# Kernel tuning notes

Measured on AMD Instinct MI355X. Metric: run time of the kernel, lower is better.

## Reference

```python
import jax, jax.numpy as jnp
import numpy as np

N = 50000
F = 128
E = 800000
HOP = 3
ALPHA = 0.2  # leaky relu slope


def setup_inputs() -> dict:
    key = jax.random.key(0)
    ks = jax.random.split(key, 6)
    x = jax.random.normal(ks[0], (N, F), dtype=jnp.float32)
    h0 = jax.random.normal(ks[1], (N, F), dtype=jnp.float32)
    edge_index = jax.random.randint(ks[2], (2, E), 0, N, dtype=jnp.int32)
    edge_weight = jax.random.uniform(ks[3], (E,), dtype=jnp.float32)
    # xavier-uniform-ish params
    lim_w = float(np.sqrt(6.0 / (F + F)))
    W_att = jax.random.uniform(ks[4], (F, F), dtype=jnp.float32, minval=-lim_w, maxval=lim_w)
    lim_a = 1.414 * float(np.sqrt(6.0 / (2 * F + 1)))
    a = jax.random.uniform(ks[5], (2 * F, 1), dtype=jnp.float32, minval=-lim_a, maxval=lim_a)
    temp = jnp.zeros((4,), dtype=jnp.float32)
    return {"x": x, "h0": h0, "edge_index": edge_index, "edge_weight": edge_weight,
            "W_att": W_att, "a": a, "temp": temp}


def _segment_softmax(e, rows, num_segments):
    m = jax.ops.segment_max(e, rows, num_segments=num_segments)
    m = jnp.where(jnp.isfinite(m), m, 0.0)  # guard empty rows
    ex = jnp.exp(e - m[rows])
    s = jax.ops.segment_sum(ex, rows, num_segments=num_segments)
    s = jnp.where(s > 0, s, 1.0)
    return ex / s[rows]


def reference(x, h0, edge_index, edge_weight, W_att, a, temp):
    rows, cols = edge_index[0], edge_index[1]
    # --- attention (edge-wise, never materializing dense NxN e) ---
    feat = x @ W_att                       # [N, F]
    f1 = (feat @ a[:F]).squeeze(-1)        # [N]
    f2 = (feat @ a[F:]).squeeze(-1)        # [N]
    e = f1[rows] + f2[cols]                # e[i,j] at edges
    e = jnp.where(e > 0, e, ALPHA * e)     # leaky relu
    att = _segment_softmax(e, rows, N)     # sparse row softmax values
    P = 0.5 * att
    # --- lifting bases ---
    coe = jax.nn.sigmoid(temp)
    rowsum = jax.ops.segment_sum(edge_weight * P, rows, num_segments=N)  # [N]
    update = x
    feat_prime = None
    for step in range(HOP):
        # sparse mm: U @ update
        update = jax.ops.segment_sum(att[:, None] * update[cols], rows, num_segments=N)
        feat_even = coe[0] * x + update
        feat_odd = update - feat_even * rowsum[:, None]
        feat_prime = feat_odd if step == 0 else coe[2] * feat_prime + (1.0 - coe[2]) * feat_odd
    return feat_prime
```

## Files before the change

### kernel.cpp

```cpp
#include <hip/hip_runtime.h>
#include <hip/hip_fp16.h>

#define NN 50000
#define FF 128
#define EE 800000
#define CAP 48
#define ALPHA 0.2f
#define ESHIFT 4.0f

__global__ void k_w(const float* __restrict__ W, const float* __restrict__ a,
                    float* __restrict__ w12) {
    int k = threadIdx.x;
    float s1 = 0.f, s2 = 0.f;
    const float* wr = W + k * FF;
    for (int j = 0; j < FF; ++j) {
        float w = wr[j];
        s1 += w * a[j];
        s2 += w * a[FF + j];
    }
    w12[k] = s1;
    w12[FF + k] = s2;
}

__global__ void k_f(const float* __restrict__ x, const float* __restrict__ w12,
                    float* __restrict__ f1, float* __restrict__ f2,
                    __half* __restrict__ xh) {
    int gid = blockIdx.x * blockDim.x + threadIdx.x;
    int node = gid >> 6;
    int lane = threadIdx.x & 63;
    if (node >= NN) return;
    float2 xv = ((const float2*)(x + (size_t)node * FF))[lane];
    ((__half2*)(xh + (size_t)node * FF))[lane] = __float22half2_rn(xv);
    float2 w1 = ((const float2*)w12)[lane];
    float2 w2 = ((const float2*)(w12 + FF))[lane];
    float s1 = xv.x * w1.x + xv.y * w1.y;
    float s2 = xv.x * w2.x + xv.y * w2.y;
#pragma unroll
    for (int o = 32; o > 0; o >>= 1) {
        s1 += __shfl_down(s1, o);
        s2 += __shfl_down(s2, o);
    }
    if (lane == 0) { f1[node] = s1; f2[node] = s2; }
}

__global__ void k_edge(const int* __restrict__ rows, const int* __restrict__ cols,
                       const float* __restrict__ ew, const float* __restrict__ f1,
                       const float* __restrict__ f2, int* __restrict__ fill,
                       int2* __restrict__ bucket) {
    const int STR = EE / 4;
    int t = blockIdx.x * blockDim.x + threadIdx.x;
    if (t >= STR) return;
    int r[4], c[4];
    float w[4];
#pragma unroll
    for (int k = 0; k < 4; ++k) {
        int e = t + k * STR;
        r[k] = rows[e];
        c[k] = cols[e];
        w[k] = ew[e];
    }
    float f1v[4], f2v[4];
#pragma unroll
    for (int k = 0; k < 4; ++k) { f1v[k] = f1[r[k]]; f2v[k] = f2[c[k]]; }
    int pay[4];
#pragma unroll
    for (int k = 0; k < 4; ++k) {
        float v = f1v[k] + f2v[k];
        v = v > 0.f ? v : ALPHA * v;
        float ex = __expf(v - ESHIFT);
        union { int i; __half2 h; } p;
        p.h = __floats2half2_rn(ex, w[k] * ex);
        pay[k] = p.i;
    }
    int pos[4];
#pragma unroll
    for (int k = 0; k < 4; ++k) pos[k] = atomicAdd(&fill[r[k]], 1);
#pragma unroll
    for (int k = 0; k < 4; ++k) {
        if (pos[k] < CAP)
            bucket[(size_t)r[k] * CAP + pos[k]] = make_int2(c[k], pay[k]);
    }
}

__global__ void k_hop(const float* __restrict__ x, const __half* __restrict__ uin,
                      __half* __restrict__ uout, const int* __restrict__ fill,
                      const int2* __restrict__ bucket, const float* __restrict__ temp,
                      __half* __restrict__ S, float* __restrict__ out, int step) {
    int wave = threadIdx.x >> 6;
    int lane = threadIdx.x & 63;
    int r = __builtin_amdgcn_readfirstlane(blockIdx.x * 4 + wave);
    if (r >= NN) return;
    int d = fill[r];
    if (d > CAP) d = CAP;
    const int2* bk = bucket + (size_t)r * CAP;
    float ax = 0.f, ay = 0.f, se = 0.f, sw = 0.f;
    int j = 0;
    for (; j + 8 <= d; j += 8) {
        int2 b[8];
        __half2 h[8];
#pragma unroll
        for (int t = 0; t < 8; ++t) b[t] = bk[j + t];
#pragma unroll
        for (int t = 0; t < 8; ++t)
            h[t] = ((const __half2*)(uin + (size_t)b[t].x * FF))[lane];
#pragma unroll
        for (int t = 0; t < 8; ++t) {
            union { int i; __half2 h2; } p;
            p.i = b[t].y;
            float2 ee = __half22float2(p.h2);
            float2 u = __half22float2(h[t]);
            ax += ee.x * u.x;
            ay += ee.x * u.y;
            se += ee.x;
            sw += ee.y;
        }
    }
    for (; j < d; ++j) {
        int2 b = bk[j];
        __half2 hv = ((const __half2*)(uin + (size_t)b.x * FF))[lane];
        union { int i; __half2 h2; } p;
        p.i = b.y;
        float2 ee = __half22float2(p.h2);
        float2 u = __half22float2(hv);
        ax += ee.x * u.x;
        ay += ee.x * u.y;
        se += ee.x;
        sw += ee.y;
    }
    float inv = se > 0.f ? 1.f / se : 0.f;
    ax *= inv;
    ay *= inv;
    float c2 = 1.f / (1.f + __expf(-temp[2]));
    __half2* Sr = (__half2*)(S + (size_t)r * FF);
    if (step == 0) {
        ((__half2*)(uout + (size_t)r * FF))[lane] = __float22half2_rn(make_float2(ax, ay));
        float w0 = c2 * c2;
        Sr[lane] = __float22half2_rn(make_float2(w0 * ax, w0 * ay));
    } else if (step == 1) {
        ((__half2*)(uout + (size_t)r * FF))[lane] = __float22half2_rn(make_float2(ax, ay));
        float w1 = c2 * (1.f - c2);
        float2 sv = __half22float2(Sr[lane]);
        Sr[lane] = __float22half2_rn(make_float2(sv.x + w1 * ax, sv.y + w1 * ay));
    } else {
        float rs = 0.5f * sw * inv;
        float coe0 = 1.f / (1.f + __expf(-temp[0]));
        float w2 = 1.f - c2;
        float2 sv = __half22float2(Sr[lane]);
        float2 xv = ((const float2*)(x + (size_t)r * FF))[lane];
        float k1 = 1.f - rs;
        float k2 = coe0 * rs;
        ((float2*)(out + (size_t)r * FF))[lane] =
            make_float2(k1 * (sv.x + w2 * ax) - k2 * xv.x,
                        k1 * (sv.y + w2 * ay) - k2 * xv.y);
    }
}

extern "C" void kernel_launch(void* const* d_in, const int* in_sizes, int n_in,
                              void* d_out, int out_size, void* d_ws, size_t ws_size,
                              hipStream_t stream) {
    const float* x = (const float*)d_in[0];
    const int* eidx = (const int*)d_in[2];
    const int* rows = eidx;
    const int* cols = eidx + EE;
    const float* ew = (const float*)d_in[3];
    const float* W = (const float*)d_in[4];
    const float* a = (const float*)d_in[5];
    const float* temp = (const float*)d_in[6];
    float* out = (float*)d_out;

    float* ws = (float*)d_ws;
    int* fill = (int*)ws;
    float* f1 = ws + NN;
    float* f2 = ws + 2 * NN;
    float* w12 = ws + 3 * NN;
    int2* bucket = (int2*)(ws + 3 * NN + 256);
    __half* xh = (__half*)(bucket + (size_t)NN * CAP);
    __half* uh0 = xh + (size_t)NN * FF;
    __half* Sb = uh0 + (size_t)NN * FF;
    __half* uh1 = xh;

    hipMemsetAsync(fill, 0, NN * sizeof(int), stream);

    k_w<<<1, 128, 0, stream>>>(W, a, w12);
    k_f<<<(NN + 3) / 4, 256, 0, stream>>>(x, w12, f1, f2, xh);
    k_edge<<<(EE / 4 + 255) / 256, 256, 0, stream>>>(rows, cols, ew, f1, f2, fill, bucket);
    k_hop<<<(NN + 3) / 4, 256, 0, stream>>>(x, xh, uh0, fill, bucket, temp, Sb, out, 0);
    k_hop<<<(NN + 3) / 4, 256, 0, stream>>>(x, uh0, uh1, fill, bucket, temp, Sb, out, 1);
    k_hop<<<(NN + 3) / 4, 256, 0, stream>>>(x, uh1, nullptr, fill, bucket, temp, Sb, out, 2);
}
```

Baseline: 283.9 us.

## Build compact CSR via two-level binning instead of per-row atomic buckets

Result: faster. 258.4 us (-9.0%).

```diff
diff --git a/kernel.cpp b/kernel.cpp
--- a/kernel.cpp
+++ b/kernel.cpp
@@ -4,9 +4,13 @@
 #define NN 50000
 #define FF 128
 #define EE 800000
-#define CAP 48
 #define ALPHA 0.2f
 #define ESHIFT 4.0f
+
+#define NBINS 196
+#define RPB 256
+#define CAPB 5120
+#define EPB 2048
 
 __global__ void k_w(const float* __restrict__ W, const float* __restrict__ a,
                     float* __restrict__ w12) {
@@ -43,56 +47,122 @@
     if (lane == 0) { f1[node] = s1; f2[node] = s2; }
 }
 
-__global__ void k_edge(const int* __restrict__ rows, const int* __restrict__ cols,
-                       const float* __restrict__ ew, const float* __restrict__ f1,
-                       const float* __restrict__ f2, int* __restrict__ fill,
-                       int2* __restrict__ bucket) {
-    const int STR = EE / 4;
-    int t = blockIdx.x * blockDim.x + threadIdx.x;
-    if (t >= STR) return;
-    int r[4], c[4];
-    float w[4];
-#pragma unroll
-    for (int k = 0; k < 4; ++k) {
-        int e = t + k * STR;
-        r[k] = rows[e];
-        c[k] = cols[e];
-        w[k] = ew[e];
-    }
-    float f1v[4], f2v[4];
-#pragma unroll
-    for (int k = 0; k < 4; ++k) { f1v[k] = f1[r[k]]; f2v[k] = f2[c[k]]; }
-    int pay[4];
-#pragma unroll
-    for (int k = 0; k < 4; ++k) {
-        float v = f1v[k] + f2v[k];
-        v = v > 0.f ? v : ALPHA * v;
-        float ex = __expf(v - ESHIFT);
-        union { int i; __half2 h; } p;
-        p.h = __floats2half2_rn(ex, w[k] * ex);
-        pay[k] = p.i;
-    }
-    int pos[4];
-#pragma unroll
-    for (int k = 0; k < 4; ++k) pos[k] = atomicAdd(&fill[r[k]], 1);
-#pragma unroll
-    for (int k = 0; k < 4; ++k) {
-        if (pos[k] < CAP)
-            bucket[(size_t)r[k] * CAP + pos[k]] = make_int2(c[k], pay[k]);
-    }
+__global__ void k_bin(const int* __restrict__ rows, const int* __restrict__ cols,
+                      const float* __restrict__ ew, const float* __restrict__ f1,
+                      const float* __restrict__ f2, int* __restrict__ bin_fill,
+                      int2* __restrict__ binbuf) {
+    __shared__ int cnt[NBINS];
+    __shared__ int gbase[NBINS];
+    int tid = threadIdx.x;
+    if (tid < NBINS) cnt[tid] = 0;
+    __syncthreads();
+    int e0 = blockIdx.x * EPB;
+    int rk[8], bn[8], rc[8], pay[8];
+    bool vl[8];
+#pragma unroll
+    for (int k = 0; k < 8; ++k) {
+        int e = e0 + k * 256 + tid;
+        vl[k] = e < EE;
+        if (vl[k]) {
+            int r = rows[e], c = cols[e];
+            float v = f1[r] + f2[c];
+            v = v > 0.f ? v : ALPHA * v;
+            float ex = __expf(v - ESHIFT);
+            union { int i; __half2 h; } p;
+            p.h = __floats2half2_rn(ex, ew[e] * ex);
+            pay[k] = p.i;
+            rc[k] = (r << 16) | c;
+            bn[k] = r >> 8;
+            rk[k] = atomicAdd(&cnt[bn[k]], 1);
+        }
+    }
+    __syncthreads();
+    if (tid < NBINS) {
+        int c0 = cnt[tid];
+        gbase[tid] = c0 ? atomicAdd(&bin_fill[tid], c0) : 0;
+    }
+    __syncthreads();
+#pragma unroll
+    for (int k = 0; k < 8; ++k) {
+        if (vl[k]) {
+            int pos = gbase[bn[k]] + rk[k];
+            if (pos < CAPB) binbuf[(size_t)bn[k] * CAPB + pos] = make_int2(rc[k], pay[k]);
+        }
+    }
+}
+
+__global__ void k_csr(const int* __restrict__ bin_fill, const int2* __restrict__ binbuf,
+                      int2* __restrict__ csr, int* __restrict__ row_ptr) {
+    __shared__ int sc[256];
+    __shared__ int lfill[RPB];
+    __shared__ int2 grouped[CAPB];
+    int tid = threadIdx.x;
+    int bin = blockIdx.x;
+    if (tid < 256) {
+        int v = (tid < NBINS) ? bin_fill[tid] : 0;
+        sc[tid] = v > CAPB ? CAPB : v;
+    }
+    __syncthreads();
+    for (int s = 1; s < 256; s <<= 1) {
+        int t = 0;
+        if (tid < 256) t = sc[tid] + (tid >= s ? sc[tid - s] : 0);
+        __syncthreads();
+        if (tid < 256) sc[tid] = t;
+        __syncthreads();
+    }
+    int base = (bin > 0) ? sc[bin - 1] : 0;
+    int cnt = sc[bin] - base;
+    __syncthreads();
+    if (tid < RPB) lfill[tid] = 0;
+    __syncthreads();
+    int2 ent[5];
+    int rnk[5], rl[5];
+    bool vl[5];
+#pragma unroll
+    for (int it = 0; it < 5; ++it) {
+        int i = tid + it * 1024;
+        vl[it] = i < cnt;
+        if (vl[it]) {
+            ent[it] = binbuf[(size_t)bin * CAPB + i];
+            rl[it] = (((unsigned)ent[it].x) >> 16) & 0xFF;
+            rnk[it] = atomicAdd(&lfill[rl[it]], 1);
+        }
+    }
+    __syncthreads();
+    if (tid < 256) sc[tid] = lfill[tid];
+    __syncthreads();
+    for (int s = 1; s < 256; s <<= 1) {
+        int t = 0;
+        if (tid < 256) t = sc[tid] + (tid >= s ? sc[tid - s] : 0);
+        __syncthreads();
+        if (tid < 256) sc[tid] = t;
+        __syncthreads();
+    }
+#pragma unroll
+    for (int it = 0; it < 5; ++it) {
+        if (vl[it])
+            grouped[sc[rl[it]] - lfill[rl[it]] + rnk[it]] =
+                make_int2(ent[it].x & 0xFFFF, ent[it].y);
+    }
+    __syncthreads();
+    for (int i = tid; i < cnt; i += 1024) csr[base + i] = grouped[i];
+    int r0 = bin << 8;
+    int nrows = NN - r0 < RPB ? NN - r0 : RPB;
+    if (tid < nrows) row_ptr[r0 + tid] = base + sc[tid] - lfill[tid];
+    if (bin == NBINS - 1 && tid == 0) row_ptr[NN] = base + cnt;
 }
 
 __global__ void k_hop(const float* __restrict__ x, const __half* __restrict__ uin,
-                      __half* __restrict__ uout, const int* __restrict__ fill,
-                      const int2* __restrict__ bucket, const float* __restrict__ temp,
+                      __half* __restrict__ uout, const int* __restrict__ row_ptr,
+                      const int2* __restrict__ csr, const float* __restrict__ temp,
                       __half* __restrict__ S, float* __restrict__ out, int step) {
     int wave = threadIdx.x >> 6;
     int lane = threadIdx.x & 63;
     int r = __builtin_amdgcn_readfirstlane(blockIdx.x * 4 + wave);
     if (r >= NN) return;
-    int d = fill[r];
-    if (d > CAP) d = CAP;
-    const int2* bk = bucket + (size_t)r * CAP;
+    int beg = row_ptr[r], end = row_ptr[r + 1];
+    const int2* bk = csr + beg;
+    int d = end - beg;
     float ax = 0.f, ay = 0.f, se = 0.f, sw = 0.f;
     int j = 0;
     for (; j + 8 <= d; j += 8) {
@@ -169,22 +239,25 @@
     float* out = (float*)d_out;
 
     float* ws = (float*)d_ws;
-    int* fill = (int*)ws;
-    float* f1 = ws + NN;
-    float* f2 = ws + 2 * NN;
-    float* w12 = ws + 3 * NN;
-    int2* bucket = (int2*)(ws + 3 * NN + 256);
-    __half* xh = (__half*)(bucket + (size_t)NN * CAP);
+    int* bin_fill = (int*)ws;
+    float* w12 = ws + 256;
+    float* f1 = ws + 512;
+    float* f2 = f1 + NN;
+    int* row_ptr = (int*)(f2 + NN);
+    int2* csr = (int2*)(row_ptr + NN + 64);
+    __half* xh = (__half*)(csr + EE);
     __half* uh0 = xh + (size_t)NN * FF;
     __half* Sb = uh0 + (size_t)NN * FF;
+    int2* binbuf = (int2*)Sb;
     __half* uh1 = xh;
 
-    hipMemsetAsync(fill, 0, NN * sizeof(int), stream);
+    hipMemsetAsync(bin_fill, 0, NBINS * sizeof(int), stream);
 
     k_w<<<1, 128, 0, stream>>>(W, a, w12);
     k_f<<<(NN + 3) / 4, 256, 0, stream>>>(x, w12, f1, f2, xh);
-    k_edge<<<(EE / 4 + 255) / 256, 256, 0, stream>>>(rows, cols, ew, f1, f2, fill, bucket);
-    k_hop<<<(NN + 3) / 4, 256, 0, stream>>>(x, xh, uh0, fill, bucket, temp, Sb, out, 0);
-    k_hop<<<(NN + 3) / 4, 256, 0, stream>>>(x, uh0, uh1, fill, bucket, temp, Sb, out, 1);
-    k_hop<<<(NN + 3) / 4, 256, 0, stream>>>(x, uh1, nullptr, fill, bucket, temp, Sb, out, 2);
-}
+    k_bin<<<(EE + EPB - 1) / EPB, 256, 0, stream>>>(rows, cols, ew, f1, f2, bin_fill, binbuf);
+    k_csr<<<NBINS, 1024, 0, stream>>>(bin_fill, binbuf, csr, row_ptr);
+    k_hop<<<(NN + 3) / 4, 256, 0, stream>>>(x, xh, uh0, row_ptr, csr, temp, Sb, out, 0);
+    k_hop<<<(NN + 3) / 4, 256, 0, stream>>>(x, uh0, uh1, row_ptr, csr, temp, Sb, out, 1);
+    k_hop<<<(NN + 3) / 4, 256, 0, stream>>>(x, uh1, nullptr, row_ptr, csr, temp, Sb, out, 2);
+}
```
